# Kernel tuning notes

Hardware: AMD Instinct MI355X
Metric: run time of the kernel (lower is better)

## Reference

```python
import jax, jax.numpy as jnp
import numpy as np

M_SQRT1_2 = 0.7071067811865476
P_DROP = 0.1  # activation_dropout


def setup_inputs() -> dict:
    key = jax.random.key(0)
    k1, k2, k3, k4 = jax.random.split(key, 4)
    N, FFN, EMB = 8192, 4096, 1024
    x = jax.random.normal(k1, (N, FFN), dtype=jnp.float16)
    weight = (jax.random.normal(k2, (EMB, FFN), dtype=jnp.float32) * (1.0 / np.sqrt(FFN))).astype(jnp.float16)
    bias = jax.random.normal(k3, (EMB,), dtype=jnp.float16)
    mask = jax.random.uniform(k4, (N, FFN)) >= P_DROP  # keep mask (bool)
    return {"x": x, "weight": weight, "bias": bias, "mask": mask}


def reference(x, weight, bias, mask):
    # GELU computed in fp32, cast back to fp16 (matches the custom IR)
    xf = x.astype(jnp.float32)
    g = (0.5 * xf * (1.0 + jax.lax.erf(xf * M_SQRT1_2))).astype(jnp.float16)
    # dropout: mask then scale by 1/(1-p) in fp16
    scale = jnp.float16(1.0 / (1.0 - P_DROP))
    h = g * mask.astype(jnp.float16) * scale  # [N, FFN]
    # y[N0, N2] = sum_N1 h[N0, N1] * weight[N2, N1] + bias[N2]
    y = jnp.einsum('nf,ef->ne', h, weight) + bias[None, :]
    return y
```

## Files before the change

### kernel.cpp

```cpp
#include <hip/hip_runtime.h>
#include <stdint.h>

typedef uint32_t u32;
typedef uint16_t u16;

static constexpr int M_DIM = 8192;
static constexpr int N_DIM = 1024;
static constexpr int K_DIM = 4096;

static constexpr int BM = 256;
static constexpr int BN = 128;
static constexpr int BK = 64;
static constexpr int KT64 = K_DIM / BK;
static constexpr int K_TILES32 = K_DIM / 32;
static constexpr int MB_TILES = M_DIM / 16;
static constexpr int NB_TILES = N_DIM / 16;

static constexpr size_t FRAG_U16 = 512;
static constexpr size_t HT_BYTES = (size_t)MB_TILES * K_TILES32 * FRAG_U16 * 2;
static constexpr size_t WT_BYTES = (size_t)NB_TILES * K_TILES32 * FRAG_U16 * 2;
static constexpr size_t WS_NEEDED = HT_BYTES + WT_BYTES;

typedef __attribute__((ext_vector_type(8))) _Float16 half8;
typedef __attribute__((ext_vector_type(4))) float f32x4;

__device__ __forceinline__ u32 pack2(float a, float b) {
  union { _Float16 h[2]; u32 u; } p;
  p.h[0] = (_Float16)a;
  p.h[1] = (_Float16)b;
  return p.u;
}

__device__ __forceinline__ float gelu_drop(float x, u32 keep) {
  float ax = fabsf(x);
  float z  = ax * 0.70710678f;
  float t  = __builtin_amdgcn_rcpf(fmaf(0.3275911f, z, 1.0f));
  float poly = fmaf(fmaf(fmaf(fmaf(1.061405429f, t, -1.453152027f),
                              t, 1.421413741f),
                         t, -0.284496736f),
                    t, 0.254829592f) * t;
  float e   = exp2f(z * z * -1.44269504f);
  float erf = fmaf(-poly, e, 1.0f);
  float g   = 0.5f * x * (1.0f + copysignf(erf, x));
  return keep ? g * 1.1111112f : 0.0f;
}

__device__ __forceinline__ void async_cp16(const void* g, void* l) {
  __builtin_amdgcn_global_load_lds((__attribute__((address_space(1))) u32*)g,
                                   (__attribute__((address_space(3))) u32*)l,
                                   16, 0, 0);
}

static constexpr int H_PAIRS = MB_TILES * (K_TILES32 / 2);
static constexpr int W_PAIRS = NB_TILES * (K_TILES32 / 2);
static constexpr int PACK_BLOCKS = (H_PAIRS + W_PAIRS) / 4;

__global__ __launch_bounds__(256)
void pack_kernel(const float* __restrict__ X, const int* __restrict__ Mask,
                 const float* __restrict__ W, u16* __restrict__ Ht, u16* __restrict__ Wt) {
  const int l     = threadIdx.x & 63;
  const int pi    = blockIdx.x * 4 + (threadIdx.x >> 6);
  const int row16 = l & 15;
  const int kof   = (l >> 4) << 4;

  const int fsub = kof >> 5;
  const int q0   = (kof & 31) >> 3;

  if (pi < H_PAIRS) {
    const int mb = pi >> 6, kp = pi & 63;
    const size_t src = (size_t)(mb * 16 + row16) * K_DIM + kp * 64 + kof;
    const float* xp = X    + src;
    const int*   mp = Mask + src;
    float4 x0 = *(const float4*)(xp + 0);
    float4 x1 = *(const float4*)(xp + 4);
    float4 x2 = *(const float4*)(xp + 8);
    float4 x3 = *(const float4*)(xp + 12);
    uint4  m0 = *(const uint4*)(mp + 0);
    uint4  m1 = *(const uint4*)(mp + 4);
    uint4  m2 = *(const uint4*)(mp + 8);
    uint4  m3 = *(const uint4*)(mp + 12);
    u32 o0 = pack2(gelu_drop(x0.x, m0.x), gelu_drop(x0.y, m0.y));
    u32 o1 = pack2(gelu_drop(x0.z, m0.z), gelu_drop(x0.w, m0.w));
    u32 o2 = pack2(gelu_drop(x1.x, m1.x), gelu_drop(x1.y, m1.y));
    u32 o3 = pack2(gelu_drop(x1.z, m1.z), gelu_drop(x1.w, m1.w));
    u32 o4 = pack2(gelu_drop(x2.x, m2.x), gelu_drop(x2.y, m2.y));
    u32 o5 = pack2(gelu_drop(x2.z, m2.z), gelu_drop(x2.w, m2.w));
    u32 o6 = pack2(gelu_drop(x3.x, m3.x), gelu_drop(x3.y, m3.y));
    u32 o7 = pack2(gelu_drop(x3.z, m3.z), gelu_drop(x3.w, m3.w));
    const int f = kp * 2 + fsub;
    u16* dst = Ht + (size_t)(mb * 128 + f) * FRAG_U16 + (size_t)(row16 + 16 * q0) * 8;
    *(uint4*)(dst)       = make_uint4(o0, o1, o2, o3);
    *(uint4*)(dst + 128) = make_uint4(o4, o5, o6, o7);
  } else {
    const int pj = pi - H_PAIRS;
    const int nb = pj >> 6, kp = pj & 63;
    const float* wp = W + (size_t)(nb * 16 + row16) * K_DIM + kp * 64 + kof;
    float4 w0 = *(const float4*)(wp + 0);
    float4 w1 = *(const float4*)(wp + 4);
    float4 w2 = *(const float4*)(wp + 8);
    float4 w3 = *(const float4*)(wp + 12);
    const int f = kp * 2 + fsub;
    u16* dst = Wt + (size_t)(nb * 128 + f) * FRAG_U16 + (size_t)(row16 + 16 * q0) * 8;
    *(uint4*)(dst)       = make_uint4(pack2(w0.x, w0.y), pack2(w0.z, w0.w),
                                      pack2(w1.x, w1.y), pack2(w1.z, w1.w));
    *(uint4*)(dst + 128) = make_uint4(pack2(w2.x, w2.y), pack2(w2.z, w2.w),
                                      pack2(w3.x, w3.y), pack2(w3.z, w3.w));
  }
}

__global__ __launch_bounds__(512, 1)
void gemm_kernel(const u16* __restrict__ Ht, const u16* __restrict__ Wt,
                 const float* __restrict__ Bias, float* __restrict__ Out) {
  __shared__ __attribute__((aligned(16))) u16 Abuf[3][BM * BK];
  __shared__ __attribute__((aligned(16))) u16 Bbuf[3][BN * BK];

  const int tid  = threadIdx.x;
  const int lane = tid & 63;
  const int wv   = tid >> 6;
  const int wr   = wv >> 1;
  const int wc   = wv & 1;

  const int bm = blockIdx.x & 31;
  const int bn = blockIdx.x >> 5;
  const int m0 = bm * BM;
  const int n0 = bn * BN;

  const char* aG = (const char*)Ht;
  const char* bG = (const char*)Wt;
  size_t aOff[4], bOff[2];
#pragma unroll
  for (int p = 0; p < 4; ++p) {
    const int s = tid + 512 * p, f = s >> 6;
    aOff[p] = ((size_t)(bm * 16 + (f >> 1)) * K_TILES32 + (f & 1)) * 1024 + (size_t)(s & 63) * 16;
  }
#pragma unroll
  for (int p = 0; p < 2; ++p) {
    const int s = tid + 512 * p, f = s >> 6;
    bOff[p] = ((size_t)(bn * 8 + (f >> 1)) * K_TILES32 + (f & 1)) * 1024 + (size_t)(s & 63) * 16;
  }

  auto stage = [&](int kt, int buf) {
    const size_t ko = (size_t)kt * 2048;
    char* ad = (char*)Abuf[buf];
    char* bd = (char*)Bbuf[buf];
#pragma unroll
    for (int p = 0; p < 4; ++p)
      async_cp16(aG + aOff[p] + ko, ad + (tid + 512 * p) * 16);
#pragma unroll
    for (int p = 0; p < 2; ++p)
      async_cp16(bG + bOff[p] + ko, bd + (tid + 512 * p) * 16);
  };

  f32x4 acc[4][4];
#pragma unroll
  for (int i = 0; i < 4; ++i)
#pragma unroll
    for (int j = 0; j < 4; ++j)
      acc[i][j] = (f32x4){0.f, 0.f, 0.f, 0.f};

  auto compute = [&](int buf) {
    const char* ab = (const char*)Abuf[buf];
    const char* bb = (const char*)Bbuf[buf];
#pragma unroll
    for (int kk = 0; kk < 2; ++kk) {
      half8 ar[4], br[4];
#pragma unroll
      for (int i = 0; i < 4; ++i)
        ar[i] = *(const half8*)(ab + (((wr * 4 + i) * 2 + kk) * 64 + lane) * 16);
#pragma unroll
      for (int j = 0; j < 4; ++j)
        br[j] = *(const half8*)(bb + (((wc * 4 + j) * 2 + kk) * 64 + lane) * 16);
      __builtin_amdgcn_s_setprio(1);
#pragma unroll
      for (int i = 0; i < 4; ++i)
#pragma unroll
        for (int j = 0; j < 4; ++j)
          acc[i][j] = __builtin_amdgcn_mfma_f32_16x16x32_f16(ar[i], br[j], acc[i][j], 0, 0, 0);
      __builtin_amdgcn_s_setprio(0);
    }
  };

  stage(0, 0);
  stage(1, 1);

  int cur = 0;
#pragma unroll 1
  for (int kt = 0; kt < KT64; ++kt) {
    if (kt + 2 < KT64) {
      asm volatile("s_waitcnt vmcnt(6)" ::: "memory");
      __builtin_amdgcn_s_barrier();
      asm volatile("" ::: "memory");
      stage(kt + 2, cur == 0 ? 2 : cur - 1);
    } else if (kt + 1 < KT64) {
      asm volatile("s_waitcnt vmcnt(6)" ::: "memory");
      __builtin_amdgcn_s_barrier();
      asm volatile("" ::: "memory");
    } else {
      asm volatile("s_waitcnt vmcnt(0)" ::: "memory");
      __builtin_amdgcn_s_barrier();
      asm volatile("" ::: "memory");
    }
    compute(cur);
    cur = (cur == 2) ? 0 : cur + 1;
  }

  const int fr = lane & 15;
  const int rq = (lane >> 4) << 2;
  float bv[4];
#pragma unroll
  for (int j = 0; j < 4; ++j)
    bv[j] = Bias[n0 + wc * 64 + j * 16 + fr];

#pragma unroll
  for (int i = 0; i < 4; ++i) {
    const int row0 = m0 + wr * 64 + i * 16 + rq;
#pragma unroll
    for (int j = 0; j < 4; ++j) {
      const int col = n0 + wc * 64 + j * 16 + fr;
#pragma unroll
      for (int r = 0; r < 4; ++r)
        Out[(size_t)(row0 + r) * N_DIM + col] = acc[i][j][r] + bv[j];
    }
  }
}

static constexpr int A_STRIDE = 40;

__global__ __launch_bounds__(256, 2)
void fused_fallback_kernel(const float* __restrict__ X, const float* __restrict__ W,
                           const float* __restrict__ Bias, const int* __restrict__ Mask,
                           float* __restrict__ Out) {
  __shared__ __attribute__((aligned(16))) _Float16 As[128 * A_STRIDE];
  __shared__ __attribute__((aligned(16))) _Float16 Bs[128 * 32];

  const int tid  = threadIdx.x;
  const int lane = tid & 63;
  const int wv   = tid >> 6;
  const int wr   = wv >> 1;
  const int wc   = wv & 1;
  const int bm = blockIdx.x & 63;
  const int bn = blockIdx.x >> 6;
  const int m0 = bm * 128;
  const int n0 = bn * 128;

  const int a_m = tid >> 1;
  const int a_k = (tid & 1) << 4;
  const float* xptr = X    + (size_t)(m0 + a_m) * K_DIM + a_k;
  const int*   mptr = Mask + (size_t)(m0 + a_m) * K_DIM + a_k;
  _Float16* a_lds = &As[a_m * A_STRIDE + a_k];

  const int i0 = tid, i1 = tid + 256;
  const float* wp0 = W + (size_t)(n0 + (i0 >> 2)) * K_DIM + ((i0 & 3) << 3);
  const float* wp1 = W + (size_t)(n0 + (i1 >> 2)) * K_DIM + ((i1 & 3) << 3);
  _Float16* bl0 = &Bs[i0 * 8];
  _Float16* bl1 = &Bs[i1 * 8];

  f32x4 acc[4][4];
#pragma unroll
  for (int i = 0; i < 4; ++i)
#pragma unroll
    for (int j = 0; j < 4; ++j)
      acc[i][j] = (f32x4){0.f, 0.f, 0.f, 0.f};

  float4 xf0 = *(const float4*)(xptr +  0);
  float4 xf1 = *(const float4*)(xptr +  4);
  float4 xf2 = *(const float4*)(xptr +  8);
  float4 xf3 = *(const float4*)(xptr + 12);
  uint4  mr0 = *(const uint4*)(mptr +  0);
  uint4  mr1 = *(const uint4*)(mptr +  4);
  uint4  mr2 = *(const uint4*)(mptr +  8);
  uint4  mr3 = *(const uint4*)(mptr + 12);
  float4 wf0 = *(const float4*)(wp0 + 0);
  float4 wf1 = *(const float4*)(wp0 + 4);
  float4 wf2 = *(const float4*)(wp1 + 0);
  float4 wf3 = *(const float4*)(wp1 + 4);

#pragma unroll 1
  for (int kt = 0; kt < 128; ++kt) {
    {
      float xs[16] = {xf0.x, xf0.y, xf0.z, xf0.w, xf1.x, xf1.y, xf1.z, xf1.w,
                      xf2.x, xf2.y, xf2.z, xf2.w, xf3.x, xf3.y, xf3.z, xf3.w};
      u32 mk[16]   = {mr0.x, mr0.y, mr0.z, mr0.w, mr1.x, mr1.y, mr1.z, mr1.w,
                      mr2.x, mr2.y, mr2.z, mr2.w, mr3.x, mr3.y, mr3.z, mr3.w};
      u32 ow[8];
#pragma unroll
      for (int e = 0; e < 8; ++e)
        ow[e] = pack2(gelu_drop(xs[2 * e], mk[2 * e]), gelu_drop(xs[2 * e + 1], mk[2 * e + 1]));
      ((uint4*)a_lds)[0] = make_uint4(ow[0], ow[1], ow[2], ow[3]);
      ((uint4*)a_lds)[1] = make_uint4(ow[4], ow[5], ow[6], ow[7]);
    }
    {
      *(uint4*)bl0 = make_uint4(pack2(wf0.x, wf0.y), pack2(wf0.z, wf0.w),
                                pack2(wf1.x, wf1.y), pack2(wf1.z, wf1.w));
      *(uint4*)bl1 = make_uint4(pack2(wf2.x, wf2.y), pack2(wf2.z, wf2.w),
                                pack2(wf3.x, wf3.y), pack2(wf3.z, wf3.w));
    }
    __syncthreads();

    if (kt + 1 < 128) {
      xptr += 32; mptr += 32; wp0 += 32; wp1 += 32;
      xf0 = *(const float4*)(xptr +  0);
      xf1 = *(const float4*)(xptr +  4);
      xf2 = *(const float4*)(xptr +  8);
      xf3 = *(const float4*)(xptr + 12);
      mr0 = *(const uint4*)(mptr +  0);
      mr1 = *(const uint4*)(mptr +  4);
      mr2 = *(const uint4*)(mptr +  8);
      mr3 = *(const uint4*)(mptr + 12);
      wf0 = *(const float4*)(wp0 + 0);
      wf1 = *(const float4*)(wp0 + 4);
      wf2 = *(const float4*)(wp1 + 0);
      wf3 = *(const float4*)(wp1 + 4);
    }

    {
      const int fr2 = lane & 15;
      const int fk2 = (lane >> 4) << 3;
      half8 ar[4], br[4];
#pragma unroll
      for (int i = 0; i < 4; ++i)
        ar[i] = *(const half8*)&As[(wr * 64 + i * 16 + fr2) * A_STRIDE + fk2];
#pragma unroll
      for (int j = 0; j < 4; ++j)
        br[j] = *(const half8*)&Bs[(wc * 64 + j * 16 + fr2) * 32 + fk2];
#pragma unroll
      for (int i = 0; i < 4; ++i)
#pragma unroll
        for (int j = 0; j < 4; ++j)
          acc[i][j] = __builtin_amdgcn_mfma_f32_16x16x32_f16(ar[i], br[j], acc[i][j], 0, 0, 0);
    }
    __syncthreads();
  }

  const int fr = lane & 15;
  const int rq = (lane >> 4) << 2;
  float bv[4];
#pragma unroll
  for (int j = 0; j < 4; ++j)
    bv[j] = Bias[n0 + wc * 64 + j * 16 + fr];
#pragma unroll
  for (int i = 0; i < 4; ++i) {
    const int row0 = m0 + wr * 64 + i * 16 + rq;
#pragma unroll
    for (int j = 0; j < 4; ++j) {
      const int col = n0 + wc * 64 + j * 16 + fr;
#pragma unroll
      for (int r = 0; r < 4; ++r)
        Out[(size_t)(row0 + r) * N_DIM + col] = acc[i][j][r] + bv[j];
    }
  }
}

extern "C" void kernel_launch(void* const* d_in, const int* in_sizes, int n_in,
                              void* d_out, int out_size, void* d_ws, size_t ws_size,
                              hipStream_t stream) {
  const float* X    = (const float*)d_in[0];
  const float* W    = (const float*)d_in[1];
  const float* Bias = (const float*)d_in[2];
  const int*   Mk   = (const int*)d_in[3];
  float* Out = (float*)d_out;

  if (ws_size >= WS_NEEDED) {
    u16* Ht = (u16*)d_ws;
    u16* Wt = (u16*)((char*)d_ws + HT_BYTES);
    pack_kernel<<<PACK_BLOCKS, 256, 0, stream>>>(X, Mk, W, Ht, Wt);
    gemm_kernel<<<(M_DIM / BM) * (N_DIM / BN), 512, 0, stream>>>(Ht, Wt, Bias, Out);
  } else {
    fused_fallback_kernel<<<64 * 8, 256, 0, stream>>>(X, W, Bias, Mk, Out);
  }
}
```

Measured before the change: 401.2 us.

## Split K-tile staging into halves interleaved with per-kk MFMA phases

The main loop is restructured into two phases per K-tile. Each phase loads its LDS fragments, issues half of the next async global-to-LDS copies, then waits and synchronises. After that comes a scheduling-fenced, high-priority block of 16 MFMAs followed by a trailing barrier. The aim is to spread global load issue across the compute and keep the MFMA stream tight by stopping the compiler from interleaving other instructions. The cost is more workgroup barriers per K-tile, which could add stall time.

```diff
diff --git a/kernel.cpp b/kernel.cpp
--- a/kernel.cpp
+++ b/kernel.cpp
@@ -139,16 +139,24 @@
     bOff[p] = ((size_t)(bn * 8 + (f >> 1)) * K_TILES32 + (f & 1)) * 1024 + (size_t)(s & 63) * 16;
   }
 
-  auto stage = [&](int kt, int buf) {
+  auto stageHalf = [&](int kt, int buf, int h) {
     const size_t ko = (size_t)kt * 2048;
     char* ad = (char*)Abuf[buf];
     char* bd = (char*)Bbuf[buf];
-#pragma unroll
-    for (int p = 0; p < 4; ++p)
-      async_cp16(aG + aOff[p] + ko, ad + (tid + 512 * p) * 16);
-#pragma unroll
-    for (int p = 0; p < 2; ++p)
-      async_cp16(bG + bOff[p] + ko, bd + (tid + 512 * p) * 16);
+    if (h == 0) {
+      async_cp16(aG + aOff[0] + ko, ad + (size_t)(tid)*16);
+      async_cp16(aG + aOff[1] + ko, ad + (size_t)(tid + 512) * 16);
+      async_cp16(bG + bOff[0] + ko, bd + (size_t)(tid)*16);
+    } else {
+      async_cp16(aG + aOff[2] + ko, ad + (size_t)(tid + 1024) * 16);
+      async_cp16(aG + aOff[3] + ko, ad + (size_t)(tid + 1536) * 16);
+      async_cp16(bG + bOff[1] + ko, bd + (size_t)(tid + 512) * 16);
+    }
+  };
+
+  auto stageFull = [&](int kt, int buf) {
+    stageHalf(kt, buf, 0);
+    stageHalf(kt, buf, 1);
   };
 
   f32x4 acc[4][4];
@@ -158,50 +166,46 @@
     for (int j = 0; j < 4; ++j)
       acc[i][j] = (f32x4){0.f, 0.f, 0.f, 0.f};
 
-  auto compute = [&](int buf) {
+  auto phase = [&](int buf, int kk, int stKt, int stBuf, int h, int vm) {
     const char* ab = (const char*)Abuf[buf];
     const char* bb = (const char*)Bbuf[buf];
-#pragma unroll
-    for (int kk = 0; kk < 2; ++kk) {
-      half8 ar[4], br[4];
-#pragma unroll
-      for (int i = 0; i < 4; ++i)
-        ar[i] = *(const half8*)(ab + (((wr * 4 + i) * 2 + kk) * 64 + lane) * 16);
+    half8 ar[4], br[4];
+#pragma unroll
+    for (int i = 0; i < 4; ++i)
+      ar[i] = *(const half8*)(ab + (size_t)(((wr * 4 + i) * 2 + kk) * 64 + lane) * 16);
+#pragma unroll
+    for (int j = 0; j < 4; ++j)
+      br[j] = *(const half8*)(bb + (size_t)(((wc * 4 + j) * 2 + kk) * 64 + lane) * 16);
+    if (stKt >= 0) stageHalf(stKt, stBuf, h);
+    if (vm == 6) asm volatile("s_waitcnt vmcnt(6)" ::: "memory");
+    else if (vm == 0) asm volatile("s_waitcnt vmcnt(0)" ::: "memory");
+    __builtin_amdgcn_s_barrier();
+    asm volatile("s_waitcnt lgkmcnt(0)" ::: "memory");
+    __builtin_amdgcn_sched_barrier(0);
+    __builtin_amdgcn_s_setprio(1);
+#pragma unroll
+    for (int i = 0; i < 4; ++i)
 #pragma unroll
       for (int j = 0; j < 4; ++j)
-        br[j] = *(const half8*)(bb + (((wc * 4 + j) * 2 + kk) * 64 + lane) * 16);
-      __builtin_amdgcn_s_setprio(1);
-#pragma unroll
-      for (int i = 0; i < 4; ++i)
-#pragma unroll
-        for (int j = 0; j < 4; ++j)
-          acc[i][j] = __builtin_amdgcn_mfma_f32_16x16x32_f16(ar[i], br[j], acc[i][j], 0, 0, 0);
-      __builtin_amdgcn_s_setprio(0);
-    }
+        acc[i][j] = __builtin_amdgcn_mfma_f32_16x16x32_f16(ar[i], br[j], acc[i][j], 0, 0, 0);
+    __builtin_amdgcn_s_setprio(0);
+    __builtin_amdgcn_sched_barrier(0);
+    __builtin_amdgcn_s_barrier();
   };
 
-  stage(0, 0);
-  stage(1, 1);
-
-  int cur = 0;
+  stageFull(0, 0);
+  stageFull(1, 1);
+  asm volatile("s_waitcnt vmcnt(6)" ::: "memory");
+  __builtin_amdgcn_s_barrier();
+
 #pragma unroll 1
   for (int kt = 0; kt < KT64; ++kt) {
-    if (kt + 2 < KT64) {
-      asm volatile("s_waitcnt vmcnt(6)" ::: "memory");
-      __builtin_amdgcn_s_barrier();
-      asm volatile("" ::: "memory");
-      stage(kt + 2, cur == 0 ? 2 : cur - 1);
-    } else if (kt + 1 < KT64) {
-      asm volatile("s_waitcnt vmcnt(6)" ::: "memory");
-      __builtin_amdgcn_s_barrier();
-      asm volatile("" ::: "memory");
-    } else {
-      asm volatile("s_waitcnt vmcnt(0)" ::: "memory");
-      __builtin_amdgcn_s_barrier();
-      asm volatile("" ::: "memory");
-    }
-    compute(cur);
-    cur = (cur == 2) ? 0 : cur + 1;
+    const int cur  = kt % 3;
+    const bool st  = (kt + 2) < KT64;
+    const int  sb  = (kt + 2) % 3;
+    const int vm = st ? 6 : ((kt + 1) < KT64 ? 0 : -1);
+    phase(cur, 0, st ? kt + 2 : -1, sb, 0, -1);
+    phase(cur, 1, st ? kt + 2 : -1, sb, 1, vm);
   }
 
   const int fr = lane & 15;
```

After: 389.0 us. -3.0%, faster.
